# Performance work log

Hardware: AMD Instinct MI355X
Metric: run time of the kernel (lower is better)

Reference implementation:

```python
import jax, jax.numpy as jnp
import numpy as np

N = 8192            # number of candidate boxes (S*S*B proposals)
NUM_CLASSES = 80    # COCO
IOU_THRESHOLD = 0.5


def setup_inputs() -> dict:
    key = jax.random.key(0)
    k1, k2, k3, k4 = jax.random.split(key, 4)
    # valid boxes: x1,y1 in [0,500), w,h in [1,101) -> x2>x1, y2>y1
    xy = jax.random.uniform(k1, (N, 2), dtype=jnp.float32) * 500.0
    wh = jax.random.uniform(k2, (N, 2), dtype=jnp.float32) * 100.0 + 1.0
    obj = jax.random.uniform(k3, (N, 1), dtype=jnp.float32)
    cls = jax.random.uniform(k4, (N, NUM_CLASSES), dtype=jnp.float32)
    X = jnp.concatenate([xy, xy + wh, obj, cls], axis=1)  # (N, 5+C)
    return {"X": X}


def reference(X):
    """Faithful jax version of torchvision.ops.batched_nms applied to YOLO output.

    Returns X reordered by descending combined score, with suppressed rows
    zeroed (fixed output shape instead of data-dependent X[nms_idx]).
    """
    cls_probs = X[:, 5:]                       # (N, C)
    score = jnp.max(cls_probs, axis=1)         # per-box best class prob
    cat = jnp.argmax(cls_probs, axis=1)        # per-box class id
    scores = X[:, 4] * score                   # objectness * class prob

    boxes = X[:, 0:4]
    # batched_nms class-offset trick: shift boxes of different classes apart
    max_coord = jnp.max(boxes)
    offsets = cat.astype(boxes.dtype) * (max_coord + 1.0)
    b = boxes + offsets[:, None]               # (N, 4)

    order = jnp.argsort(-scores)               # descending score
    b = b[order]

    # pairwise IoU, (N, N)
    area = (b[:, 2] - b[:, 0]) * (b[:, 3] - b[:, 1])           # (N,)
    lt = jnp.maximum(b[:, None, :2], b[None, :, :2])           # (N,N,2)
    rb = jnp.minimum(b[:, None, 2:], b[None, :, 2:])           # (N,N,2)
    wh = jnp.clip(rb - lt, 0.0)
    inter = wh[..., 0] * wh[..., 1]
    iou = inter / (area[:, None] + area[None, :] - inter)

    n = b.shape[0]
    idx = jnp.arange(n)

    def body(i, supp):
        # if box i survives, suppress all later boxes overlapping it
        row = (iou[i] > IOU_THRESHOLD) & (idx > i) & jnp.logical_not(supp[i])
        return supp | row

    suppressed = jax.lax.fori_loop(0, n, body, jnp.zeros((n,), dtype=bool))
    keep = jnp.logical_not(suppressed)          # (N,) mask in score order

    return X[order] * keep[:, None].astype(X.dtype)
```

## Files before the change

### kernel.cpp

```cpp
#include <hip/hip_runtime.h>


#define N 8192
#define NC 80
#define COLS 85
#define MPC 192

__global__ __launch_bounds__(256) void score_kernel(const float* __restrict__ X,
                                                    unsigned long long* __restrict__ keys,
                                                    int* __restrict__ cat,
                                                    float* __restrict__ maxarr) {
    int wave = threadIdx.x >> 6;
    int lane = threadIdx.x & 63;
    int row = blockIdx.x * 4 + wave;
    const float* rp = X + (size_t)row * COLS;

    float v1 = rp[5 + lane];
    float v2 = (lane < 16) ? rp[5 + 64 + lane] : -INFINITY;
    float bv; int bi;
    if (v2 > v1) { bv = v2; bi = lane + 64; } else { bv = v1; bi = lane; }
    #pragma unroll
    for (int m = 32; m >= 1; m >>= 1) {
        float ov = __shfl_xor(bv, m, 64);
        int   oi = __shfl_xor(bi, m, 64);
        if (ov > bv || (ov == bv && oi < bi)) { bv = ov; bi = oi; }
    }
    float c = (lane < 4) ? rp[lane] : 0.0f;
    #pragma unroll
    for (int m = 32; m >= 1; m >>= 1) c = fmaxf(c, __shfl_xor(c, m, 64));

    __shared__ float cmax[4];
    if (lane == 0) {
        float s = __fmul_rn(rp[4], bv);
        keys[row] = ((unsigned long long)__float_as_uint(s) << 13)
                  | (unsigned long long)(8191 - row);
        cat[row] = bi;
        cmax[wave] = c;
    }
    __syncthreads();
    if (threadIdx.x == 0)
        maxarr[blockIdx.x] = fmaxf(fmaxf(cmax[0], cmax[1]), fmaxf(cmax[2], cmax[3]));
}

__global__ __launch_bounds__(1024) void rank_kernel(const unsigned long long* __restrict__ keys,
                                                    int* __restrict__ rank) {
    __shared__ unsigned long long ikey[32];
    __shared__ int part[32 * 17];

    const int t    = threadIdx.x;
    const int wave = t >> 6;
    const int lane = t & 63;

    unsigned long long key[8];
    #pragma unroll
    for (int k = 0; k < 8; ++k) key[k] = keys[t + 1024 * k];
    if (t < 32) ikey[t] = keys[blockIdx.x * 32 + t];
    __syncthreads();

    unsigned long long Ki = ikey[0];
    for (int ii = 0; ii < 32; ++ii) {
        unsigned long long Kn = ikey[(ii + 1) & 31];
        int cnt = 0;
        #pragma unroll
        for (int k = 0; k < 8; ++k)
            cnt += __popcll(__ballot(key[k] > Ki));
        if (lane == 0) part[ii * 17 + wave] = cnt;
        Ki = Kn;
    }
    __syncthreads();
    if (t < 32) {
        int g = 0;
        #pragma unroll
        for (int w = 0; w < 16; ++w) g += part[t * 17 + w];
        rank[blockIdx.x * 32 + t] = g;
    }
}

__global__ __launch_bounds__(1024) void nms_out_kernel(const float* __restrict__ X,
                                                       const int* __restrict__ cat,
                                                       const int* __restrict__ rank,
                                                       const float* __restrict__ maxarr,
                                                       float* __restrict__ out) {
    __shared__ int           mrow[MPC];
    __shared__ unsigned long long bits[128];
    __shared__ int           pfx[128];
    __shared__ float4        lbox[MPC];
    __shared__ float         larea[MPC];
    __shared__ int           lrow[MPC];
    __shared__ int           lorig[MPC];
    __shared__ unsigned long long Pm[MPC][3];
    __shared__ unsigned char lkeep[MPC];
    __shared__ float         swmax[16];
    __shared__ int           mcount;

    const int t    = threadIdx.x;
    const int wave = t >> 6;
    const int lane = t & 63;
    const int c    = blockIdx.x;

    if (t == 0) mcount = 0;
    if (t < 128) bits[t] = 0ULL;

    float tm = fmaxf(maxarr[t], maxarr[t + 1024]);
    #pragma unroll
    for (int m = 32; m >= 1; m >>= 1) tm = fmaxf(tm, __shfl_xor(tm, m, 64));
    if (lane == 0) swmax[wave] = tm;

    int cat8[8];
    #pragma unroll
    for (int k = 0; k < 8; ++k) cat8[k] = cat[t + 1024 * k];
    __syncthreads();
    float gmax = swmax[0];
    #pragma unroll
    for (int w = 1; w < 16; ++w) gmax = fmaxf(gmax, swmax[w]);
    const float F = __fadd_rn(gmax, 1.0f);

    #pragma unroll
    for (int k = 0; k < 8; ++k) {
        int j = t + 1024 * k;
        int pred = (cat8[k] == c);
        unsigned long long bm = __ballot(pred);
        int old = 0;
        if (lane == 0 && bm) old = atomicAdd(&mcount, __popcll(bm));
        old = __shfl(old, 0, 64);
        if (pred) {
            int pos = old + __popcll(bm & ((1ULL << lane) - 1ULL));
            if (pos < MPC) mrow[pos] = j;
        }
    }
    __syncthreads();
    int M = mcount < MPC ? mcount : MPC;
    if (M == 0) return;

    int g = 0, orig = 0;
    if (t < M) {
        orig = mrow[t];
        g = rank[orig];
        atomicOr(&bits[g >> 6], 1ULL << (g & 63));
    }
    __syncthreads();

    if (t < 64) {
        int s0 = (int)__popcll(bits[lane]);
        int s1 = (int)__popcll(bits[64 + lane]);
        int x0 = s0, x1 = s1;
        #pragma unroll
        for (int d = 1; d < 64; d <<= 1) {
            int v0 = __shfl_up(x0, d, 64);
            int v1 = __shfl_up(x1, d, 64);
            if (lane >= d) { x0 += v0; x1 += v1; }
        }
        int tot0 = __shfl(x0, 63, 64);
        pfx[lane]      = x0 - s0;
        pfx[64 + lane] = x1 - s1 + tot0;
    }
    __syncthreads();

    if (t < M) {
        int w = g >> 6;
        int cr = pfx[w] + (int)__popcll(bits[w] & ((1ULL << (g & 63)) - 1ULL));
        const float* rp = X + (size_t)orig * COLS;
        float off = __fmul_rn((float)c, F);
        float b0 = __fadd_rn(rp[0], off);
        float b1 = __fadd_rn(rp[1], off);
        float b2 = __fadd_rn(rp[2], off);
        float b3 = __fadd_rn(rp[3], off);
        lbox[cr]  = make_float4(b0, b1, b2, b3);
        larea[cr] = __fmul_rn(__fsub_rn(b2, b0), __fsub_rn(b3, b1));
        lrow[cr]  = g;
        lorig[cr] = orig;
    }
    __syncthreads();

    float4 mbox[3]; float marea[3];
    #pragma unroll
    for (int s = 0; s < 3; ++s) {
        int j = (s << 6) + lane;
        if (j < M) { mbox[s] = lbox[j]; marea[s] = larea[j]; }
        else       { mbox[s] = make_float4(0.f, 0.f, 0.f, 0.f); marea[s] = 0.f; }
    }

    for (int i = wave; i < M; i += 16) {
        float4 cb = lbox[i];
        float  ca = larea[i];
        unsigned long long w0, w1, w2;
        #pragma unroll
        for (int s = 0; s < 3; ++s) {
            int j = (s << 6) + lane;
            int pred = 0;
            if (j > i && j < M) {
                float ltx = fmaxf(cb.x, mbox[s].x), lty = fmaxf(cb.y, mbox[s].y);
                float rbx = fminf(cb.z, mbox[s].z), rby = fminf(cb.w, mbox[s].w);
                float wx = fmaxf(__fsub_rn(rbx, ltx), 0.0f);
                float wy = fmaxf(__fsub_rn(rby, lty), 0.0f);
                float inter = __fmul_rn(wx, wy);
                float denom = __fsub_rn(__fadd_rn(ca, marea[s]), inter);
                float iou = __fdiv_rn(inter, denom);
                pred = (iou > 0.5f) ? 1 : 0;
            }
            unsigned long long bm = __ballot(pred);
            if (s == 0) w0 = bm; else if (s == 1) w1 = bm; else w2 = bm;
        }
        if (lane == 0) { Pm[i][0] = w0; Pm[i][1] = w1; Pm[i][2] = w2; }
    }
    __syncthreads();

    if (t < 64) {
        unsigned long long r0 = 0, r1 = 0, r2 = 0;
        unsigned long long p0 = Pm[0][0], p1 = Pm[0][1], p2 = Pm[0][2];
        #pragma unroll 4
        for (int i = 0; i < M; ++i) {
            int ip = (i + 1 < M) ? i + 1 : i;
            unsigned long long q0 = Pm[ip][0], q1 = Pm[ip][1], q2 = Pm[ip][2];
            unsigned long long cur = (i < 64) ? r0 : ((i < 128) ? r1 : r2);
            if (((cur >> (i & 63)) & 1ULL) == 0ULL) {
                r0 |= p0; r1 |= p1; r2 |= p2;
            }
            p0 = q0; p1 = q1; p2 = q2;
        }
        if (lane < M)       lkeep[lane]       = (unsigned char)((r0 >> lane) & 1ULL);
        if (64 + lane < M)  lkeep[64 + lane]  = (unsigned char)((r1 >> lane) & 1ULL);
        if (128 + lane < M) lkeep[128 + lane] = (unsigned char)((r2 >> lane) & 1ULL);
    }
    __syncthreads();

    for (int m = wave; m < M; m += 16) {
        float keepf = lkeep[m] ? 0.0f : 1.0f;
        const float* src = X + (size_t)lorig[m] * COLS;
        float*       dst = out + (size_t)lrow[m] * COLS;
        float v0 = src[lane];
        float v1 = (lane < COLS - 64) ? src[64 + lane] : 0.0f;
        dst[lane] = __fmul_rn(v0, keepf);
        if (lane < COLS - 64) dst[64 + lane] = __fmul_rn(v1, keepf);
    }
}

extern "C" void kernel_launch(void* const* d_in, const int* in_sizes, int n_in,
                              void* d_out, int out_size, void* d_ws, size_t ws_size,
                              hipStream_t stream) {
    const float* X = (const float*)d_in[0];
    float* out = (float*)d_out;
    char* ws = (char*)d_ws;

    unsigned long long* keys = (unsigned long long*)(ws + 0);
    int*   cat    = (int*)(ws + 65536);
    float* maxarr = (float*)(ws + 98304);
    int*   rank   = (int*)(ws + 106496);

    score_kernel<<<N / 4, 256, 0, stream>>>(X, keys, cat, maxarr);
    rank_kernel<<<N / 32, 1024, 0, stream>>>(keys, rank);
    nms_out_kernel<<<NC, 1024, 0, stream>>>(X, cat, rank, maxarr, out);
}
```

Baseline: 86.95 us.

## Split output gather into a separate fully parallel kernel via keep map

The per-class NMS kernel now writes a compact map from output row to source row plus a suppression flag, instead of copying rows itself. A new kernel spread over the whole GPU then gathers and zeroes the output, one element per thread. The aim is to move the large output copy off the 80-block NMS launch, where each block copied its rows slowly with one wave per row. The cost is an extra launch and a small workspace round trip.

```diff
diff --git a/kernel.cpp b/kernel.cpp
--- a/kernel.cpp
+++ b/kernel.cpp
@@ -76,11 +76,11 @@
     }
 }
 
-__global__ __launch_bounds__(1024) void nms_out_kernel(const float* __restrict__ X,
-                                                       const int* __restrict__ cat,
-                                                       const int* __restrict__ rank,
-                                                       const float* __restrict__ maxarr,
-                                                       float* __restrict__ out) {
+__global__ __launch_bounds__(1024) void nms_kernel(const float* __restrict__ X,
+                                                   const int* __restrict__ cat,
+                                                   const int* __restrict__ rank,
+                                                   const float* __restrict__ maxarr,
+                                                   unsigned int* __restrict__ kmap) {
     __shared__ int           mrow[MPC];
     __shared__ unsigned long long bits[128];
     __shared__ int           pfx[128];
@@ -89,7 +89,6 @@
     __shared__ int           lrow[MPC];
     __shared__ int           lorig[MPC];
     __shared__ unsigned long long Pm[MPC][3];
-    __shared__ unsigned char lkeep[MPC];
     __shared__ float         swmax[16];
     __shared__ int           mcount;
 
@@ -205,6 +204,7 @@
     }
     __syncthreads();
 
+    __shared__ unsigned long long rsup[3];
     if (t < 64) {
         unsigned long long r0 = 0, r1 = 0, r2 = 0;
         unsigned long long p0 = Pm[0][0], p1 = Pm[0][1], p2 = Pm[0][2];
@@ -218,21 +218,29 @@
             }
             p0 = q0; p1 = q1; p2 = q2;
         }
-        if (lane < M)       lkeep[lane]       = (unsigned char)((r0 >> lane) & 1ULL);
-        if (64 + lane < M)  lkeep[64 + lane]  = (unsigned char)((r1 >> lane) & 1ULL);
-        if (128 + lane < M) lkeep[128 + lane] = (unsigned char)((r2 >> lane) & 1ULL);
-    }
-    __syncthreads();
-
-    for (int m = wave; m < M; m += 16) {
-        float keepf = lkeep[m] ? 0.0f : 1.0f;
-        const float* src = X + (size_t)lorig[m] * COLS;
-        float*       dst = out + (size_t)lrow[m] * COLS;
-        float v0 = src[lane];
-        float v1 = (lane < COLS - 64) ? src[64 + lane] : 0.0f;
-        dst[lane] = __fmul_rn(v0, keepf);
-        if (lane < COLS - 64) dst[64 + lane] = __fmul_rn(v1, keepf);
-    }
+        if (lane == 0) { rsup[0] = r0; rsup[1] = r1; rsup[2] = r2; }
+    }
+    __syncthreads();
+
+    if (t < M) {
+        int cr = 0;
+        {
+        }
+        cr = t;
+        unsigned long long sup = (rsup[cr >> 6] >> (cr & 63)) & 1ULL;
+        kmap[lrow[cr]] = (unsigned int)lorig[cr] | (sup ? 0x80000000u : 0u);
+    }
+}
+
+__global__ __launch_bounds__(1024) void out_kernel(const float* __restrict__ X,
+                                                   const unsigned int* __restrict__ kmap,
+                                                   float* __restrict__ out) {
+    int idx = blockIdx.x * 1024 + threadIdx.x;
+    int r = idx / COLS;
+    int col = idx - r * COLS;
+    unsigned int v = kmap[r];
+    float f = (v & 0x80000000u) ? 0.0f : 1.0f;
+    out[idx] = __fmul_rn(X[(size_t)(v & 0x1FFFu) * COLS + col], f);
 }
 
 extern "C" void kernel_launch(void* const* d_in, const int* in_sizes, int n_in,
@@ -243,11 +251,13 @@
     char* ws = (char*)d_ws;
 
     unsigned long long* keys = (unsigned long long*)(ws + 0);
-    int*   cat    = (int*)(ws + 65536);
-    float* maxarr = (float*)(ws + 98304);
-    int*   rank   = (int*)(ws + 106496);
+    int*          cat    = (int*)(ws + 65536);
+    float*        maxarr = (float*)(ws + 98304);
+    int*          rank   = (int*)(ws + 106496);
+    unsigned int* kmap   = (unsigned int*)(ws + 139264);
 
     score_kernel<<<N / 4, 256, 0, stream>>>(X, keys, cat, maxarr);
     rank_kernel<<<N / 32, 1024, 0, stream>>>(keys, rank);
-    nms_out_kernel<<<NC, 1024, 0, stream>>>(X, cat, rank, maxarr, out);
-}
+    nms_kernel<<<NC, 1024, 0, stream>>>(X, cat, rank, maxarr, kmap);
+    out_kernel<<<(N * COLS) / 1024, 1024, 0, stream>>>(X, kmap, out);
+}
```

New measurement: 85.38 us. Within noise of the previous version (-1.8%).
